# Performance work log

Hardware: AMD Instinct MI355X
Metric: run time of the kernel (lower is better)

## Reference

```python
import jax, jax.numpy as jnp
import numpy as np

ALPHA = 1.0
NEG = -1e20  # matches torch code's -1e+20 padding for impossible cells


def setup_inputs() -> dict:
    key = jax.random.key(0)
    W = jax.random.normal(key, (32, 512, 1024), dtype=jnp.float32)
    return {"W": W}


def _combine(x, y):
    # associative operator for the log-space linear recurrence
    # m_j = logaddexp(m_{j-1} + a_j, b_j)
    a1, b1 = x
    a2, b2 = y
    return (a1 + a2, jnp.logaddexp(b1 + a2, b2))


def _forward(W):
    # Faithful to BayesianDTW.compute_location / compute_location_new:
    #   mu[:,0,:] = mu[:,:,0] = -1e20, mu[:,0,0] = 0
    #   mu[i,j] = logsumexp(mu[i-1,j], mu[i,j-1], mu[i-1,j-1]) + alpha*W[i-1,j-1]
    # Implemented as a row scan; the within-row left-neighbor dependency is a
    # log-space linear recurrence solved with an associative scan (O(Na*log Nb)
    # depth instead of O(Na*Nb) sequential steps).
    B, Na, Nb = W.shape
    aW = ALPHA * W  # [B, Na, Nb]
    row0 = jnp.concatenate(
        [jnp.zeros((B, 1), W.dtype), jnp.full((B, Nb), NEG, W.dtype)], axis=1
    )  # mu[:, 0, :]

    def step(prev_row, w_row):
        # prev_row: mu[:, i-1, :] -> [B, Nb+1]; w_row: alpha*W[:, i-1, :] -> [B, Nb]
        c = jnp.logaddexp(prev_row[:, 1:], prev_row[:, :-1])  # top + top-left
        # mu[i,j] = logaddexp(mu[i,j-1] + w_j, c_j + w_j), mu[i,0] = NEG
        A, Bc = jax.lax.associative_scan(_combine, (w_row, c + w_row), axis=1)
        m = jnp.logaddexp(NEG + A, Bc)  # include mu[i,0] = NEG initial carry
        new_row = jnp.concatenate(
            [jnp.full((m.shape[0], 1), NEG, m.dtype), m], axis=1
        )
        return new_row, new_row

    _, rows = jax.lax.scan(step, row0, jnp.transpose(aW, (1, 0, 2)))  # [Na, B, Nb+1]
    mu = jnp.concatenate([row0[:, None, :], jnp.transpose(rows, (1, 0, 2))], axis=1)
    return mu  # [B, Na+1, Nb+1], scale=False behavior


def reference(W):
    return _forward(W)
```

## Files before the change

### kernel.cpp

```cpp
#include <hip/hip_runtime.h>
#include <stdint.h>
#include <stddef.h>


#define NBATCH  32
#define NA      512
#define NB      1024
#define NSTRIPE 8
#define SW      128
#define CH      16
#define NCHUNK  (NA / CH)
#define LSTR    128
#define OROWS   513
#define OCOLS   1025
#define FSTRIDE 32

#define NEGV    (-1e20f)
#define LOG2E   (1.4426950408889634f)
#define LN2     (0.6931471805599453f)
#define NEG2    (-1.4426950408889634e20f)
#define FLAGTAG 0x5A000000u

#define EXP2F(x) __builtin_amdgcn_exp2f(x)
#define LOG2F(x) __builtin_amdgcn_logf(x)

__device__ __forceinline__ float lse3_2(float a, float b, float c) {
    float m = fmaxf(fmaxf(a, b), c);
    float s = EXP2F(a - m) + EXP2F(b - m) + EXP2F(c - m);
    return m + LOG2F(s);
}

__device__ __forceinline__ float rdlane(float v, int l) {
    return __int_as_float(__builtin_amdgcn_readlane(__float_as_int(v), l));
}

__device__ __forceinline__ float lane_shr1(float x, int lane) {
    int xi  = __float_as_int(x);
    int shr = __builtin_amdgcn_update_dpp(0, xi, 0x111, 0xf, 0xf, true);
    float v = __int_as_float(shr);
    float a15 = rdlane(x, 15), a31 = rdlane(x, 31), a47 = rdlane(x, 47);
    v = (lane == 16) ? a15 : v;
    v = (lane == 32) ? a31 : v;
    v = (lane == 48) ? a47 : v;
    return v;
}

__device__ __forceinline__ unsigned int ld_flag(unsigned int* fp) {
    return __hip_atomic_load(fp, __ATOMIC_RELAXED, __HIP_MEMORY_SCOPE_AGENT);
}
__device__ __forceinline__ void st_flag(unsigned int* fp, unsigned int v) {
    __hip_atomic_store(fp, v, __ATOMIC_RELAXED, __HIP_MEMORY_SCOPE_AGENT);
}
__device__ __forceinline__ float ld_edge(const float* p) {
    return __hip_atomic_load((float*)p, __ATOMIC_RELAXED, __HIP_MEMORY_SCOPE_AGENT);
}
__device__ __forceinline__ void st_edge(float* p, float v) {
    __hip_atomic_store(p, v, __ATOMIC_RELAXED, __HIP_MEMORY_SCOPE_AGENT);
}

__device__ __forceinline__ void wait_flag(unsigned int* fp, unsigned int need) {
    for (int k = 0; k < (1 << 22); ++k) {
        unsigned int v = ld_flag(fp);
        if ((v >> 24) == 0x5Au && (v & 0x00FFFFFFu) >= need) break;
    }
    asm volatile("" ::: "memory");
}

__global__ __launch_bounds__(64, 1)
void dtw_pipe(const float* __restrict__ W, float* __restrict__ out,
              unsigned int* __restrict__ flags)
{
    __shared__ float lds_w[128 * LSTR];
    __shared__ float lds_o[128 * LSTR];

    const int lane = (int)threadIdx.x;
    const int bid  = (int)blockIdx.x;
    const int b    = bid & (NBATCH - 1);
    const int s    = bid >> 5;

    const float*  Wb  = W + ((size_t)b * NA) * NB + s * SW;
    float*        ob  = out + (size_t)b * OROWS * OCOLS;
    unsigned int* fmy = flags + (size_t)bid * FSTRIDE;
    unsigned int* fup = flags + (size_t)(bid - NBATCH) * FSTRIDE;

    {
        float4 z4 = make_float4(0.f, 0.f, 0.f, 0.f);
        float4* dst = (float4*)&lds_w[48 * LSTR];
        for (int i = lane; i < (80 * LSTR) / 4; i += 64) dst[i] = z4;
    }

    ob[s * SW + 1 + lane]      = NEGV;
    ob[s * SW + 1 + 64 + lane] = NEGV;
    if (s == 0) {
        if (lane == 0) ob[0] = 0.0f;
        for (int r = lane; r < NA; r += 64)
            ob[(size_t)(r + 1) * OCOLS] = NEGV;
    }

    float2 wst[CH];
    float2 wst1[CH];
    #pragma unroll
    for (int rr = 0; rr < CH; ++rr)
        wst[rr]  = *(const float2*)(Wb + (size_t)rr * NB + 2 * lane);
    #pragma unroll
    for (int rr = 0; rr < CH; ++rr)
        wst1[rr] = *(const float2*)(Wb + (size_t)(CH + rr) * NB + 2 * lane);

    float evcur = -1e30f, evnxt = -1e30f, lres = -1e30f;
    if (s > 0) {
        wait_flag(fup, 1u);
        if (lane < CH)
            evcur = ld_edge(&ob[(size_t)(1 + lane) * OCOLS + s * SW]) * LOG2E;
        wait_flag(fup, 2u);
        if (lane < CH)
            evnxt = ld_edge(&ob[(size_t)(CH + 1 + lane) * OCOLS + s * SW]) * LOG2E;
        wait_flag(fup, 3u);
        if (lane < CH)
            lres  = ld_edge(&ob[(size_t)(2 * CH + 1 + lane) * OCOLS + s * SW]) * LOG2E;
    }

    asm volatile("s_waitcnt vmcnt(0)" ::: "memory");

    #pragma unroll
    for (int rr = 0; rr < CH; ++rr)
        *(float2*)&lds_w[rr * LSTR + 2 * lane] = wst[rr];
    #pragma unroll
    for (int rr = 0; rr < CH; ++rr)
        *(float2*)&lds_w[(CH + rr) * LSTR + 2 * lane] = wst1[rr];
    #pragma unroll
    for (int rr = 0; rr < CH; ++rr)
        wst[rr] = *(const float2*)(Wb + (size_t)(2 * CH + rr) * NB + 2 * lane);

    float topA = NEG2, topB = NEG2;
    float sh_in = NEG2;
    float tl_reg = NEG2;
    float ev_im1 = (s == 0) ? 0.0f : NEG2;
    unsigned int fpoll = 0;

    float2 w_cur = *(const float2*)&lds_w[((0 - lane) & 127) * LSTR + 2 * lane];
    float2 w_nx1 = *(const float2*)&lds_w[((1 - lane) & 127) * LSTR + 2 * lane];

    auto step = [&](int m_, int tt) {
        const int t = (m_ << 4) + tt;
        const int r = t - lane;
        if (tt == 1 && s > 0) fpoll = ld_flag(fup);
        float2 w_pre = *(const float2*)&lds_w[((r + 2) & 127) * LSTR + 2 * lane];
        const float ev_i = rdlane(evcur, tt);
        const float lf = (lane == 0) ? ev_i   : sh_in;
        const float tl = (lane == 0) ? ev_im1 : tl_reg;
        const float uA = fmaf(w_cur.x, LOG2E, lse3_2(topA, lf, tl));
        const float uB = fmaf(w_cur.y, LOG2E, lse3_2(topB, uA, topA));
        const bool on = (r >= 0);
        if (on & (r < NA)) {
            *(float2*)&lds_o[(r & 127) * LSTR + 2 * lane]
                = make_float2(uA * LN2, uB * LN2);
        }
        topA   = on ? uA : NEG2;
        topB   = on ? uB : NEG2;
        tl_reg = on ? lf : NEG2;
        ev_im1 = ev_i;
        sh_in  = lane_shr1(uB, lane);
        w_cur = w_nx1; w_nx1 = w_pre;
    };

    for (int m = 0; m < 35; ++m) {
        #pragma unroll
        for (int tt = 0; tt < 16; ++tt) step(m, tt);

        const int f = m - 4;
        if (s < NSTRIPE - 1 && f >= 0 && lane < CH) {
            const int rw = (f << 4) + lane;
            const float evl = lds_o[(rw & 127) * LSTR + 127];
            st_edge(ob + (size_t)(rw + 1) * OCOLS + (s + 1) * SW, evl);
        }
        asm volatile("s_waitcnt vmcnt(1)" ::: "memory");
        if (s < NSTRIPE - 1 && f >= 1 && lane == 0)
            st_flag(fmy, FLAGTAG + (unsigned)f);
        {
            const int cw = m + 2;
            if (cw < NCHUNK) {
                #pragma unroll
                for (int rr = 0; rr < CH; ++rr) {
                    const int slot = ((cw << 4) + rr) & 127;
                    *(float2*)&lds_w[slot * LSTR + 2 * lane] = wst[rr];
                }
            }
        }
        if (f >= 0) {
            #pragma unroll
            for (int rr = 0; rr < CH; ++rr) {
                const int rw = (f << 4) + rr;
                const float v0 = lds_o[(rw & 127) * LSTR + lane];
                const float v1 = lds_o[(rw & 127) * LSTR + 64 + lane];
                float* orow = ob + (size_t)(rw + 1) * OCOLS + s * SW + 1;
                orow[lane]      = v0;
                orow[64 + lane] = v1;
            }
        }
        evcur = evnxt; evnxt = lres;
        const int c = m + 3;
        if (s > 0 && c < NCHUNK) {
            const unsigned need = (unsigned)(m + 4);
            if (!((fpoll >> 24) == 0x5Au && (fpoll & 0x00FFFFFFu) >= need))
                wait_flag(fup, need);
            lres = -1e30f;
            if (lane < CH)
                lres = ld_edge(&ob[(size_t)((c << 4) + 1 + lane) * OCOLS + s * SW])
                       * LOG2E;
        }
        if (c < NCHUNK) {
            const float* wsrc = Wb + (size_t)(c << 4) * NB;
            #pragma unroll
            for (int rr = 0; rr < CH; ++rr)
                wst[rr] = *(const float2*)(wsrc + (size_t)rr * NB + 2 * lane);
        }
    }

    #pragma unroll
    for (int tt = 0; tt < 15; ++tt) step(35, tt);

    {
        const int f = NCHUNK - 1;
        if (s < NSTRIPE - 1 && lane < CH) {
            const int rw = (f << 4) + lane;
            const float evl = lds_o[(rw & 127) * LSTR + 127];
            st_edge(ob + (size_t)(rw + 1) * OCOLS + (s + 1) * SW, evl);
        }
        asm volatile("s_waitcnt vmcnt(1)" ::: "memory");
        if (s < NSTRIPE - 1 && lane == 0)
            st_flag(fmy, FLAGTAG + (unsigned)(NCHUNK - 1));
        #pragma unroll
        for (int rr = 0; rr < CH; ++rr) {
            const int rw = (f << 4) + rr;
            const float v0 = lds_o[(rw & 127) * LSTR + lane];
            const float v1 = lds_o[(rw & 127) * LSTR + 64 + lane];
            float* orow = ob + (size_t)(rw + 1) * OCOLS + s * SW + 1;
            orow[lane]      = v0;
            orow[64 + lane] = v1;
        }
        asm volatile("s_waitcnt vmcnt(0)" ::: "memory");
        if (s < NSTRIPE - 1 && lane == 0)
            st_flag(fmy, FLAGTAG + (unsigned)NCHUNK);
    }
}

extern "C" void kernel_launch(void* const* d_in, const int* in_sizes, int n_in,
                              void* d_out, int out_size, void* d_ws, size_t ws_size,
                              hipStream_t stream) {
    const float*  W     = (const float*)d_in[0];
    float*        out   = (float*)d_out;
    unsigned int* flags = (unsigned int*)d_ws;
    (void)in_sizes; (void)n_in; (void)out_size; (void)ws_size;
    hipLaunchKernelGGL(dtw_pipe, dim3(NBATCH * NSTRIPE), dim3(64), 0, stream,
                       W, out, flags);
}
```

Measured before the change: 419.4 us.

## Store DTW results directly to global, drop LDS output staging

Each wavefront step now writes its float2 result straight to global memory along the anti-diagonal, and lane 63 emits the stripe edge value immediately. This replaces the LDS output buffer and the per-chunk coalesced row copy-out. The inter-stripe flag is published one chunk earlier, and the W prefetch is deepened by one step to hide LDS latency. The cost is uncoalesced, strided global stores on the critical recurrence path, and flag correctness now depends on how vmcnt ordering interacts with those scattered stores.

```diff
diff --git a/kernel.cpp b/kernel.cpp
--- a/kernel.cpp
+++ b/kernel.cpp
@@ -71,7 +71,6 @@
               unsigned int* __restrict__ flags)
 {
     __shared__ float lds_w[128 * LSTR];
-    __shared__ float lds_o[128 * LSTR];
 
     const int lane = (int)threadIdx.x;
     const int bid  = (int)blockIdx.x;
@@ -139,12 +138,16 @@
 
     float2 w_cur = *(const float2*)&lds_w[((0 - lane) & 127) * LSTR + 2 * lane];
     float2 w_nx1 = *(const float2*)&lds_w[((1 - lane) & 127) * LSTR + 2 * lane];
+    float2 w_nx2 = *(const float2*)&lds_w[((2 - lane) & 127) * LSTR + 2 * lane];
+
+    float* obase = ob + s * SW + 1 + 2 * lane;
+    int    ooff  = (1 - lane) * OCOLS;
 
     auto step = [&](int m_, int tt) {
         const int t = (m_ << 4) + tt;
         const int r = t - lane;
         if (tt == 1 && s > 0) fpoll = ld_flag(fup);
-        float2 w_pre = *(const float2*)&lds_w[((r + 2) & 127) * LSTR + 2 * lane];
+        float2 w_pre = *(const float2*)&lds_w[((r + 3) & 127) * LSTR + 2 * lane];
         const float ev_i = rdlane(evcur, tt);
         const float lf = (lane == 0) ? ev_i   : sh_in;
         const float tl = (lane == 0) ? ev_im1 : tl_reg;
@@ -152,30 +155,30 @@
         const float uB = fmaf(w_cur.y, LOG2E, lse3_2(topB, uA, topA));
         const bool on = (r >= 0);
         if (on & (r < NA)) {
-            *(float2*)&lds_o[(r & 127) * LSTR + 2 * lane]
-                = make_float2(uA * LN2, uB * LN2);
+            float* op = obase + (ptrdiff_t)ooff;
+            *(float2*)op = make_float2(uA * LN2, uB * LN2);
+            if ((s < NSTRIPE - 1) & (lane == 63))
+                st_edge(op + 1, uB * LN2);
         }
         topA   = on ? uA : NEG2;
         topB   = on ? uB : NEG2;
         tl_reg = on ? lf : NEG2;
         ev_im1 = ev_i;
         sh_in  = lane_shr1(uB, lane);
-        w_cur = w_nx1; w_nx1 = w_pre;
+        w_cur = w_nx1; w_nx1 = w_nx2; w_nx2 = w_pre;
+        ooff += OCOLS;
     };
 
     for (int m = 0; m < 35; ++m) {
         #pragma unroll
         for (int tt = 0; tt < 16; ++tt) step(m, tt);
 
-        const int f = m - 4;
-        if (s < NSTRIPE - 1 && f >= 0 && lane < CH) {
-            const int rw = (f << 4) + lane;
-            const float evl = lds_o[(rw & 127) * LSTR + 127];
-            st_edge(ob + (size_t)(rw + 1) * OCOLS + (s + 1) * SW, evl);
-        }
         asm volatile("s_waitcnt vmcnt(1)" ::: "memory");
-        if (s < NSTRIPE - 1 && f >= 1 && lane == 0)
-            st_flag(fmy, FLAGTAG + (unsigned)f);
+        {
+            const int p = m - 3;
+            if (s < NSTRIPE - 1 && p >= 1 && lane == 0)
+                st_flag(fmy, FLAGTAG + (unsigned)p);
+        }
         {
             const int cw = m + 2;
             if (cw < NCHUNK) {
@@ -184,17 +187,6 @@
                     const int slot = ((cw << 4) + rr) & 127;
                     *(float2*)&lds_w[slot * LSTR + 2 * lane] = wst[rr];
                 }
-            }
-        }
-        if (f >= 0) {
-            #pragma unroll
-            for (int rr = 0; rr < CH; ++rr) {
-                const int rw = (f << 4) + rr;
-                const float v0 = lds_o[(rw & 127) * LSTR + lane];
-                const float v1 = lds_o[(rw & 127) * LSTR + 64 + lane];
-                float* orow = ob + (size_t)(rw + 1) * OCOLS + s * SW + 1;
-                orow[lane]      = v0;
-                orow[64 + lane] = v1;
             }
         }
         evcur = evnxt; evnxt = lres;
@@ -219,29 +211,9 @@
     #pragma unroll
     for (int tt = 0; tt < 15; ++tt) step(35, tt);
 
-    {
-        const int f = NCHUNK - 1;
-        if (s < NSTRIPE - 1 && lane < CH) {
-            const int rw = (f << 4) + lane;
-            const float evl = lds_o[(rw & 127) * LSTR + 127];
-            st_edge(ob + (size_t)(rw + 1) * OCOLS + (s + 1) * SW, evl);
-        }
-        asm volatile("s_waitcnt vmcnt(1)" ::: "memory");
-        if (s < NSTRIPE - 1 && lane == 0)
-            st_flag(fmy, FLAGTAG + (unsigned)(NCHUNK - 1));
-        #pragma unroll
-        for (int rr = 0; rr < CH; ++rr) {
-            const int rw = (f << 4) + rr;
-            const float v0 = lds_o[(rw & 127) * LSTR + lane];
-            const float v1 = lds_o[(rw & 127) * LSTR + 64 + lane];
-            float* orow = ob + (size_t)(rw + 1) * OCOLS + s * SW + 1;
-            orow[lane]      = v0;
-            orow[64 + lane] = v1;
-        }
-        asm volatile("s_waitcnt vmcnt(0)" ::: "memory");
-        if (s < NSTRIPE - 1 && lane == 0)
-            st_flag(fmy, FLAGTAG + (unsigned)NCHUNK);
-    }
+    asm volatile("s_waitcnt vmcnt(0)" ::: "memory");
+    if (s < NSTRIPE - 1 && lane == 0)
+        st_flag(fmy, FLAGTAG + (unsigned)NCHUNK);
 }
 
 extern "C" void kernel_launch(void* const* d_in, const int* in_sizes, int n_in,
```

Measured after the change: 425.5 us. About the same (+1.5%).
